# Kernel optimization log

Measured on AMD Instinct MI355X. Metric: run time of the kernel, lower is better.

## Reference

```python
import jax, jax.numpy as jnp
from jax import lax
import numpy as np

# ---- init hyperparameters (from init_kwargs) ----
STRIDE = 1
DP_CHANNELS = 1
ATOM_R = 8
ATOM_C = 8
NUMB_ATOM = 128
T_SC = 3
K = 256
BATCH = 32
IMG = 64


def setup_inputs() -> dict:
    key = jax.random.key(0)
    k1, k2 = jax.random.split(key)
    Y = jax.random.normal(k1, (BATCH, DP_CHANNELS, IMG, IMG), dtype=jnp.float32)
    # ConvTranspose2d weight layout: (numb_atom, dp_channels, atom_c, atom_r)
    W = jax.random.normal(k2, (NUMB_ATOM, DP_CHANNELS, ATOM_C, ATOM_R), dtype=jnp.float32)
    # normalise_weights(): each (i, j) filter divided by its L2 norm
    W = W / jnp.sqrt(jnp.sum(W ** 2, axis=(2, 3), keepdims=True))
    return {"Y": Y, "W_D": W}


def _conv_D(X, W):
    # PyTorch ConvTranspose2d (stride=1, no padding): full convolution with
    # spatially-flipped kernel; W is (in=numb_atom, out=dp_channels, kh, kw).
    kh, kw = W.shape[2], W.shape[3]
    return lax.conv_general_dilated(
        X, jnp.flip(W, (2, 3)), (1, 1),
        [(kh - 1, kh - 1), (kw - 1, kw - 1)],
        dimension_numbers=('NCHW', 'IOHW', 'NCHW'))


def _conv_Dt(R, Wt):
    # PyTorch Conv2d (VALID, stride=1): Wt is (out=numb_atom, in=dp, kh, kw)
    return lax.conv_general_dilated(
        R, Wt, (1, 1), 'VALID', dimension_numbers=('NCHW', 'OIHW', 'NCHW'))


def _hard_threshold_k(X, k):
    # keep the k largest-|.| entries per sample (over flattened C,H,W)
    B = X.shape[0]
    flat = X.reshape(B, -1)
    _, idx = lax.top_k(jnp.abs(flat), k)                      # [B, k]
    vals = jnp.take_along_axis(flat, idx, axis=1)             # [B, k]
    out = jnp.zeros_like(flat).at[jnp.arange(B)[:, None], idx].set(vals)
    return out.reshape(X.shape)


def _linesearch(Y, X, W, Wt, k):
    R = Y - _conv_D(X, W)
    g = _conv_Dt(R, Wt)
    l2_start = jnp.sum(R ** 2)

    def attempt(alpha):
        Xu = _hard_threshold_k(X + alpha * g, k)
        err = jnp.sum((Y - _conv_D(Xu, W)) ** 2)
        return Xu, err

    Xu0, err0 = attempt(jnp.float32(1.0))

    def cond(s):
        _, _, err, count = s
        return (err >= l2_start) & (count <= 15)

    def body(s):
        alpha, _, _, count = s
        alpha = alpha * jnp.float32(0.5)
        Xu, err = attempt(alpha)
        return (alpha, Xu, err, count + 1)

    alpha, Xu, err, _ = lax.while_loop(
        cond, body, (jnp.float32(1.0), Xu0, err0, jnp.int32(0)))
    return Xu, err, alpha


def reference(Y, W_D):
    # D_trans.weight = D.weight.permute(0,1,3,2) -> (numb_atom, dp, atom_r, atom_c)
    Wt = jnp.swapaxes(W_D, 2, 3)
    kh, kw = Wt.shape[2], Wt.shape[3]
    B, _, H, W_sp = Y.shape
    X = jnp.zeros((B, W_D.shape[0], H - kh + 1, W_sp - kw + 1), dtype=Y.dtype)
    for _ in range(T_SC):
        X, _, _ = _linesearch(Y, X, W_D, Wt, K)
    return X
```

## Files before the change

### kernel.cpp

```cpp
#include <hip/hip_runtime.h>
#include <stdint.h>

#define NB   32
#define NCH  128
#define IMG  64
#define IMG2 4096
#define OH   57
#define OHW  3249
#define CHW  415872
#define KTOP 256
#define NATT 17
#define NS   32
#define SCAP 512
#define NCAP 1536
#define NBUCK 8192
#define HSHIFT 18
#define TGT  512
#define RSTRIDE 72
#define NZB  257
#define BMW  12996

typedef unsigned long long ull;

__global__ void k_init(int* support_cnt) {
    if (threadIdx.x < NB) support_cnt[threadIdx.x] = 0;
}

__global__ __launch_bounds__(256) void k_resid(
    const float* __restrict__ Y, const float* __restrict__ W,
    const int* __restrict__ support_cnt, const uint32_t* __restrict__ support_idx,
    const float* __restrict__ support_val, float* __restrict__ Rg, double* __restrict__ l2part,
    uint32_t* __restrict__ hist, int* __restrict__ cand_cnt)
{
    int bx = blockIdx.x, tid = threadIdx.x;
    if (bx >= NB) {
        int zb = bx - NB;
        if (zb < 256) {
            ((uint4*)hist)[zb * 256 + tid] = make_uint4(0u, 0u, 0u, 0u);
        } else {
            ((uint4*)cand_cnt)[tid] = make_uint4(0u, 0u, 0u, 0u);
        }
        return;
    }
    int b = bx;
    __shared__ float Rs[IMG2];
    const float4* Y4 = (const float4*)(Y + b * IMG2);
    float4* R4 = (float4*)Rs;
    for (int i = tid; i < IMG2 / 4; i += 256) R4[i] = Y4[i];
    __syncthreads();
    int n = support_cnt[b];
    for (int task = tid; task < n * 64; task += 256) {
        int i = task >> 6, tap = task & 63, p = tap >> 3, q = tap & 7;
        uint32_t idx = support_idx[b * KTOP + i];
        float val = support_val[b * KTOP + i];
        int c = idx / OHW, rem = idx % OHW, s = rem / OH, t = rem % OH;
        float w = W[c * 64 + p * 8 + q];
        atomicAdd(&Rs[(s + p) * IMG + (t + q)], -val * w);
    }
    __syncthreads();
    double acc = 0.0;
    for (int i = tid; i < IMG2; i += 256) {
        float v = Rs[i];
        Rg[b * IMG2 + i] = v;
        acc += (double)v * (double)v;
    }
    __shared__ double red[256];
    red[tid] = acc; __syncthreads();
    for (int s2 = 128; s2 > 0; s2 >>= 1) { if (tid < s2) red[tid] += red[tid + s2]; __syncthreads(); }
    if (tid == 0) l2part[b] = red[0];
}

__global__ __launch_bounds__(256) void k_conv(
    const float* __restrict__ Rg, const float* __restrict__ W,
    float* __restrict__ g_out, uint32_t* __restrict__ hist)
{
    int b = blockIdx.x, cg0 = blockIdx.y, tid = threadIdx.x;
    __shared__ float Rs[71 * 72];
    __shared__ uint32_t hl[NBUCK];
    for (int i = tid; i < 71 * 72; i += 256) Rs[i] = 0.f;
    for (int i = tid; i < NBUCK; i += 256) hl[i] = 0u;
    __syncthreads();
    const float4* R4 = (const float4*)(Rg + b * IMG2);
    for (int i = tid; i < 1024; i += 256) {
        int row = i >> 4, col4 = (i & 15) * 4;
        *(float4*)&Rs[row * 72 + col4] = R4[i];
    }
    __syncthreads();
    int csub = tid >> 7;
    int tile = tid & 127;
    bool active = tile < 120;
    int tr = active ? tile / 15 : 0;
    int tc = active ? tile % 15 : 0;
    int s0 = tr * 8, t0 = tc * 4;

    for (int sub = 0; sub < 4; ++sub) {
        int c = cg0 * 8 + sub * 2 + csub;
        int c_s = __builtin_amdgcn_readfirstlane(c);
        const float* Wc = W + c_s * 64;

        float acc[8][4];
#pragma unroll
        for (int r = 0; r < 8; ++r)
#pragma unroll
            for (int cc = 0; cc < 4; ++cc) acc[r][cc] = 0.f;

#pragma unroll
        for (int rho = 0; rho < 15; ++rho) {
            float rb[12];
            const float* rp = &Rs[(s0 + rho) * 72 + t0];
            *(float4*)&rb[0] = *(const float4*)rp;
            *(float4*)&rb[4] = *(const float4*)(rp + 4);
            *(float4*)&rb[8] = *(const float4*)(rp + 8);
#pragma unroll
            for (int r = 0; r < 8; ++r) {
                const int p = rho - r;
                if (p >= 0 && p < 8) {
#pragma unroll
                    for (int q = 0; q < 8; ++q) {
                        float wv = Wc[q * 8 + p];
#pragma unroll
                        for (int cc = 0; cc < 4; ++cc)
                            acc[r][cc] = fmaf(rb[cc + q], wv, acc[r][cc]);
                    }
                }
            }
        }
        if (active) {
            float* go = g_out + (size_t)(b * NCH + c) * OHW;
#pragma unroll
            for (int r = 0; r < 8; ++r) {
                int s = s0 + r;
                if (s < OH) {
#pragma unroll
                    for (int cc = 0; cc < 4; ++cc) {
                        int t = t0 + cc;
                        if (t < OH) {
                            float v = acc[r][cc];
                            go[s * OH + t] = v;
                            uint32_t bits = __float_as_uint(v) & 0x7fffffffu;
                            atomicAdd(&hl[bits >> HSHIFT], 1u);
                        }
                    }
                }
            }
        }
    }
    __syncthreads();
    for (int i = tid; i < NBUCK; i += 256) {
        uint32_t v = hl[i];
        if (v) atomicAdd(&hist[b * NBUCK + i], v);
    }
}

__global__ __launch_bounds__(256) void k_thresh(const uint32_t* __restrict__ hist,
                                                uint32_t* __restrict__ thr) {
    int b = blockIdx.x, tid = threadIdx.x;
    uint32_t h[32];
    uint32_t s = 0;
    const uint32_t* hb = hist + b * NBUCK + tid * 32;
#pragma unroll
    for (int k = 0; k < 32; ++k) { h[k] = hb[k]; s += h[k]; }
    __shared__ uint32_t buf[2][256];
    int cur = 0;
    buf[0][tid] = s;
    __syncthreads();
    for (int d = 1; d < 256; d <<= 1) {
        uint32_t v = buf[cur][tid];
        if (tid + d < 256) v += buf[cur][tid + d];
        buf[cur ^ 1][tid] = v;
        cur ^= 1;
        __syncthreads();
    }
    uint32_t sufme = buf[cur][tid];
    uint32_t base  = (tid < 255) ? buf[cur][tid + 1] : 0u;
    if (tid == 0 && buf[cur][0] < TGT) thr[b] = 0u;
    if (base < TGT && sufme >= TGT) {
        uint32_t acc = base; int bk = 0;
#pragma unroll
        for (int k = 31; k >= 0; --k) {
            acc += h[k];
            if (acc >= TGT) { bk = tid * 32 + k; break; }
        }
        thr[b] = (uint32_t)bk << HSHIFT;
    }
}

__global__ __launch_bounds__(256) void k_collect(
    const float* __restrict__ g, const uint32_t* __restrict__ thr,
    int* __restrict__ cand_cnt, uint32_t* __restrict__ cand_idx, float* __restrict__ cand_g)
{
    int b = blockIdx.y;
    int i4 = blockIdx.x * 256 + threadIdx.x;
    if (i4 >= CHW / 4) return;
    int slice = blockIdx.x & (NS - 1);
    uint32_t tb = thr[b];
    float4 v4 = ((const float4*)(g + (size_t)b * CHW))[i4];
    float vv[4] = { v4.x, v4.y, v4.z, v4.w };
#pragma unroll
    for (int k = 0; k < 4; ++k) {
        uint32_t bits = __float_as_uint(vv[k]) & 0x7fffffffu;
        if (bits >= tb) {
            int pos = atomicAdd(&cand_cnt[b * NS + slice], 1);
            if (pos < SCAP) {
                cand_idx[(b * NS + slice) * SCAP + pos] = (uint32_t)(i4 * 4 + k);
                cand_g[(b * NS + slice) * SCAP + pos] = vv[k];
            }
        }
    }
}

__global__ __launch_bounds__(1024) void k_suppg(
    const float* __restrict__ g,
    const int* __restrict__ support_cnt, const uint32_t* __restrict__ support_idx,
    const int* __restrict__ cand_cnt, const uint32_t* __restrict__ cand_idx,
    const float* __restrict__ cand_g,
    uint32_t* __restrict__ ns_idx, float* __restrict__ ns_g, uint32_t* __restrict__ ns_pk,
    float* __restrict__ sup_g, uint32_t* __restrict__ sup_pk)
{
    int b = blockIdx.x, tid = threadIdx.x, lane = tid & 63;
    __shared__ uint32_t bm[BMW];
    __shared__ int cnts[NS];
    __shared__ ull ck[NCAP];
    __shared__ float cg_l[NCAP];
    __shared__ int nns_sh;
    int n = support_cnt[b];
    for (int i = tid; i < BMW / 4; i += 1024) ((uint4*)bm)[i] = make_uint4(0u, 0u, 0u, 0u);
    if (tid < NS) cnts[tid] = min(cand_cnt[b * NS + tid], SCAP);
    if (tid == 0) nns_sh = 0;
    __syncthreads();
    if (tid < KTOP) {
        if (tid < n) {
            uint32_t idx = support_idx[b * KTOP + tid];
            atomicOr(&bm[idx >> 5], 1u << (idx & 31));
            float gv = g[(size_t)b * CHW + idx];
            sup_g[b * KTOP + tid] = gv;
            int c = idx / OHW, r = idx % OHW, s = r / OH, t = r % OH;
            sup_pk[b * KTOP + tid] = (uint32_t)((c << 12) | (s << 6) | t);
        } else {
            sup_g[b * KTOP + tid] = 0.f;
            sup_pk[b * KTOP + tid] = 0u;
        }
    }
    __syncthreads();
    for (int t0 = tid; t0 < NS * SCAP; t0 += 1024) {
        int s = t0 >> 9, j = t0 & (SCAP - 1);
        bool keep = false; uint32_t idx = 0; float gv = 0.f;
        if (j < cnts[s]) {
            idx = cand_idx[(b * NS + s) * SCAP + j];
            gv = cand_g[(b * NS + s) * SCAP + j];
            keep = ((bm[idx >> 5] >> (idx & 31)) & 1u) == 0u;
        }
        ull mk = __ballot(keep);
        if (mk) {
            int basep = 0;
            if (lane == 0) basep = atomicAdd(&nns_sh, (int)__popcll(mk));
            basep = __shfl(basep, 0, 64);
            if (keep) {
                int p = basep + (int)__popcll(mk & ((1ull << lane) - 1ull));
                if (p < NCAP) {
                    ck[p] = ((ull)(__float_as_uint(gv) & 0x7fffffffu) << 32) | (ull)(uint32_t)(~idx);
                    cg_l[p] = gv;
                }
            }
        }
    }
    __syncthreads();
    int nns = min(nns_sh, NCAP);
    int nns8 = (nns + 7) & ~7;
    for (int i = nns + tid; i < nns8; i += 1024) ck[i] = 0ull;
    __syncthreads();
    ull myk[2]; int myr[2];
#pragma unroll
    for (int q = 0; q < 2; ++q) { int i = tid + 1024 * q; myk[q] = (i < nns) ? ck[i] : 0ull; myr[q] = 0; }
    for (int j = 0; j < nns8; j += 8) {
        ull t0 = ck[j], t1 = ck[j+1], t2 = ck[j+2], t3 = ck[j+3];
        ull t4 = ck[j+4], t5 = ck[j+5], t6 = ck[j+6], t7 = ck[j+7];
#pragma unroll
        for (int q = 0; q < 2; ++q) {
            myr[q] += ((t0 > myk[q]) ? 1 : 0) + ((t1 > myk[q]) ? 1 : 0)
                    + ((t2 > myk[q]) ? 1 : 0) + ((t3 > myk[q]) ? 1 : 0)
                    + ((t4 > myk[q]) ? 1 : 0) + ((t5 > myk[q]) ? 1 : 0)
                    + ((t6 > myk[q]) ? 1 : 0) + ((t7 > myk[q]) ? 1 : 0);
        }
    }
#pragma unroll
    for (int q = 0; q < 2; ++q) {
        int i = tid + 1024 * q;
        if (i < nns && myr[q] < KTOP) {
            uint32_t idx = ~(uint32_t)myk[q];
            int r = myr[q];
            ns_idx[b * KTOP + r] = idx;
            ns_g[b * KTOP + r] = cg_l[i];
            int c = idx / OHW, rr = idx % OHW, s = rr / OH, t = rr % OH;
            ns_pk[b * KTOP + r] = (uint32_t)((c << 12) | (s << 6) | t);
        }
    }
}

__global__ __launch_bounds__(512) void k_att2(
    const float* __restrict__ Y, const float* __restrict__ W,
    const int* __restrict__ support_cnt, const uint32_t* __restrict__ support_idx,
    const float* __restrict__ support_val,
    const float* __restrict__ sup_g, const uint32_t* __restrict__ sup_pk,
    const uint32_t* __restrict__ ns_idx, const float* __restrict__ ns_g,
    const uint32_t* __restrict__ ns_pk,
    uint32_t* __restrict__ sel_idx, float* __restrict__ sel_val, double* __restrict__ err)
{
    int a = blockIdx.x, b = blockIdx.y, tid = threadIdx.x;
    int lane = tid & 63, wid = tid >> 6;
    float alpha = ldexpf(1.f, -a);
    int n = support_cnt[b];

    __shared__ float recon[64 * RSTRIDE];
    __shared__ ull kA[KTOP];
    __shared__ ull kB[KTOP];
    __shared__ float s_v[KTOP];
    __shared__ uint32_t s_pk2[KTOP];
    __shared__ double redd[8];

    uint32_t myi = 0, mypk = 0;
    float myv = 0.f;
    ull myk = 0;
    if (tid < KTOP) {
        myi = ns_idx[b * KTOP + tid];
        myv = alpha * ns_g[b * KTOP + tid];
        mypk = ns_pk[b * KTOP + tid];
        myk = ((ull)(__float_as_uint(myv) & 0x7fffffffu) << 32) | (ull)(uint32_t)(~myi);
        kA[tid] = myk;
    } else {
        int t2 = tid - KTOP;
        if (t2 < n) {
            myi = support_idx[b * KTOP + t2];
            myv = fmaf(alpha, sup_g[b * KTOP + t2], support_val[b * KTOP + t2]);
            mypk = sup_pk[b * KTOP + t2];
        } else {
            myi = (uint32_t)(CHW + t2);
            myv = 0.f; mypk = 0u;
        }
        myk = ((ull)(__float_as_uint(myv) & 0x7fffffffu) << 32) | (ull)(uint32_t)(~myi);
        kB[t2] = myk;
    }
    for (int i = tid; i < 64 * RSTRIDE; i += 512) recon[i] = 0.f;
    __syncthreads();

    int cb = 0;
    for (int j = 0; j < KTOP; j += 8) {
        ull t0 = kB[j], t1 = kB[j+1], t2 = kB[j+2], t3 = kB[j+3];
        ull t4 = kB[j+4], t5 = kB[j+5], t6 = kB[j+6], t7 = kB[j+7];
        cb += ((t0 > myk) ? 1 : 0) + ((t1 > myk) ? 1 : 0)
            + ((t2 > myk) ? 1 : 0) + ((t3 > myk) ? 1 : 0)
            + ((t4 > myk) ? 1 : 0) + ((t5 > myk) ? 1 : 0)
            + ((t6 > myk) ? 1 : 0) + ((t7 > myk) ? 1 : 0);
    }
    int rank;
    if (tid < KTOP) {
        rank = tid + cb;
    } else {
        int lo = 0, hi = KTOP;
        while (lo < hi) { int mid = (lo + hi) >> 1; if (kA[mid] > myk) lo = mid + 1; else hi = mid; }
        rank = lo + cb;
    }
    size_t o = ((size_t)a * NB + b) * KTOP;
    if (rank < KTOP) {
        s_v[rank] = myv; s_pk2[rank] = mypk;
        sel_idx[o + rank] = myi; sel_val[o + rank] = myv;
    }
    __syncthreads();

#pragma unroll 4
    for (int task = tid; task < KTOP * 64; task += 512) {
        int i = task >> 6, tap = task & 63, p = tap >> 3, q = tap & 7;
        uint32_t pk = s_pk2[i];
        float val = s_v[i];
        int c = pk >> 12, s = (pk >> 6) & 63, t = pk & 63;
        atomicAdd(&recon[(s + p) * RSTRIDE + (t + q)], val * W[c * 64 + tap]);
    }
    __syncthreads();

    const float4* Y4 = (const float4*)(Y + b * IMG2);
    double accd = 0.0;
#pragma unroll
    for (int q2 = 0; q2 < 2; ++q2) {
        int idx = tid * 2 + q2;
        float4 y4 = Y4[idx];
        int row = idx >> 4, col = (idx & 15) * 4;
        const float* rr = &recon[row * RSTRIDE + col];
        float d0 = y4.x - rr[0]; accd += (double)d0 * (double)d0;
        float d1 = y4.y - rr[1]; accd += (double)d1 * (double)d1;
        float d2 = y4.z - rr[2]; accd += (double)d2 * (double)d2;
        float d3 = y4.w - rr[3]; accd += (double)d3 * (double)d3;
    }
    for (int d = 32; d > 0; d >>= 1) accd += __shfl_xor(accd, d, 64);
    if (lane == 0) redd[wid] = accd;
    __syncthreads();
    if (tid == 0) {
        double e = 0.0;
#pragma unroll
        for (int w2 = 0; w2 < 8; ++w2) e += redd[w2];
        err[a * NB + b] = e;
    }
}

__global__ __launch_bounds__(256) void k_update(
    const double* __restrict__ l2part, const double* __restrict__ err,
    const uint32_t* __restrict__ sel_idx, const float* __restrict__ sel_val,
    int* __restrict__ support_cnt, uint32_t* __restrict__ support_idx, float* __restrict__ support_val)
{
    int b = blockIdx.x, tid = threadIdx.x;
    __shared__ double esum[NATT + 1];
    __shared__ int sel_sh;
    if (tid < NATT) {
        double e = 0.0;
        for (int b2 = 0; b2 < NB; ++b2) e += err[tid * NB + b2];
        esum[tid] = e;
    } else if (tid == NATT) {
        double l2 = 0.0;
        for (int b2 = 0; b2 < NB; ++b2) l2 += l2part[b2];
        esum[NATT] = l2;
    }
    __syncthreads();
    if (tid == 0) {
        double l2 = esum[NATT];
        int sel = NATT - 1;
        for (int a2 = 0; a2 < NATT; ++a2) if (esum[a2] < l2) { sel = a2; break; }
        sel_sh = sel;
    }
    __syncthreads();
    int a = sel_sh;
    __shared__ uint32_t ki[KTOP];
    __shared__ float kv[KTOP];
    ki[tid] = sel_idx[((size_t)a * NB + b) * KTOP + tid];
    kv[tid] = sel_val[((size_t)a * NB + b) * KTOP + tid];
    __syncthreads();
    uint32_t me = ki[tid];
    int rank = 0;
    for (int j = 0; j < KTOP; j += 8) {
        uint32_t a0 = ki[j], a1 = ki[j+1], a2 = ki[j+2], a3 = ki[j+3];
        uint32_t a4 = ki[j+4], a5 = ki[j+5], a6 = ki[j+6], a7 = ki[j+7];
        rank += ((a0 < me) ? 1 : 0) + ((a1 < me) ? 1 : 0) + ((a2 < me) ? 1 : 0) + ((a3 < me) ? 1 : 0)
              + ((a4 < me) ? 1 : 0) + ((a5 < me) ? 1 : 0) + ((a6 < me) ? 1 : 0) + ((a7 < me) ? 1 : 0);
    }
    support_idx[b * KTOP + rank] = me;
    support_val[b * KTOP + rank] = kv[tid];
    if (tid == 0) support_cnt[b] = KTOP;
}

__global__ void k_outzero(float4* __restrict__ out) {
    int i = blockIdx.x * 256 + threadIdx.x;
    if (i < (NB * CHW) / 4) out[i] = make_float4(0.f, 0.f, 0.f, 0.f);
}

__global__ void k_scatter(const uint32_t* __restrict__ support_idx, const float* __restrict__ support_val,
                          float* __restrict__ out) {
    int b = blockIdx.x, tid = threadIdx.x;
    if (tid < KTOP) out[(size_t)b * CHW + support_idx[b * KTOP + tid]] = support_val[b * KTOP + tid];
}

static size_t align256(size_t x) { return (x + 255) & ~(size_t)255; }

extern "C" void kernel_launch(void* const* d_in, const int* in_sizes, int n_in,
                              void* d_out, int out_size, void* d_ws, size_t ws_size,
                              hipStream_t stream)
{
    const float* Y = (const float*)d_in[0];
    const float* W = (const float*)d_in[1];
    float* out = (float*)d_out;

    char* p = (char*)d_ws;
    size_t off = 0;
    auto carve = [&](size_t bytes) { void* r = p + off; off = align256(off + bytes); return r; };
    float*    Rg          = (float*)   carve(NB * IMG2 * sizeof(float));
    uint32_t* hist        = (uint32_t*)carve((size_t)NB * NBUCK * sizeof(uint32_t));
    uint32_t* thr         = (uint32_t*)carve(NB * sizeof(uint32_t));
    int*      cand_cnt    = (int*)     carve(NB * NS * sizeof(int));
    double*   l2part      = (double*)  carve(NB * sizeof(double));
    double*   err         = (double*)  carve(NATT * NB * sizeof(double));
    int*      support_cnt = (int*)     carve(NB * sizeof(int));
    uint32_t* support_idx = (uint32_t*)carve(NB * KTOP * sizeof(uint32_t));
    float*    support_val = (float*)   carve(NB * KTOP * sizeof(float));
    uint32_t* sel_idx     = (uint32_t*)carve((size_t)NATT * NB * KTOP * sizeof(uint32_t));
    float*    sel_val     = (float*)   carve((size_t)NATT * NB * KTOP * sizeof(float));
    uint32_t* cand_idx    = (uint32_t*)carve((size_t)NB * NS * SCAP * sizeof(uint32_t));
    float*    cand_g      = (float*)   carve((size_t)NB * NS * SCAP * sizeof(float));
    uint32_t* ns_idx      = (uint32_t*)carve(NB * KTOP * sizeof(uint32_t));
    float*    ns_gbuf     = (float*)   carve(NB * KTOP * sizeof(float));
    uint32_t* ns_pk       = (uint32_t*)carve(NB * KTOP * sizeof(uint32_t));
    float*    sup_gbuf    = (float*)   carve(NB * KTOP * sizeof(float));
    uint32_t* sup_pk      = (uint32_t*)carve(NB * KTOP * sizeof(uint32_t));
    (void)ws_size; (void)in_sizes; (void)n_in; (void)out_size;

    k_init<<<1, 64, 0, stream>>>(support_cnt);
    for (int t = 0; t < 3; ++t) {
        k_resid<<<NB + NZB, 256, 0, stream>>>(Y, W, support_cnt, support_idx, support_val,
                                              Rg, l2part, hist, cand_cnt);
        k_conv<<<dim3(NB, 16), 256, 0, stream>>>(Rg, W, out, hist);
        k_thresh<<<NB, 256, 0, stream>>>(hist, thr);
        k_collect<<<dim3((CHW / 4 + 255) / 256, NB), 256, 0, stream>>>(out, thr, cand_cnt, cand_idx, cand_g);
        k_suppg<<<NB, 1024, 0, stream>>>(out, support_cnt, support_idx,
                                         cand_cnt, cand_idx, cand_g,
                                         ns_idx, ns_gbuf, ns_pk, sup_gbuf, sup_pk);
        k_att2<<<dim3(NATT, NB), 512, 0, stream>>>(Y, W, support_cnt, support_idx, support_val,
                                                   sup_gbuf, sup_pk, ns_idx, ns_gbuf, ns_pk,
                                                   sel_idx, sel_val, err);
        k_update<<<NB, 256, 0, stream>>>(l2part, err, sel_idx, sel_val,
                                         support_cnt, support_idx, support_val);
    }
    k_outzero<<<((NB * CHW) / 4 + 255) / 256, 256, 0, stream>>>((float4*)out);
    k_scatter<<<NB, 256, 0, stream>>>(support_idx, support_val, out);
}
```

Measured before the change: 663.3 us.

## Pack support and candidate arrays into wide structs and reshape attempt kernel

Merges the separate index, value and packed-coordinate arrays into 64-bit and uint4 records so each element is read with one wide load. The attempt kernel also changes: the rank count uses wavefront shuffles instead of LDS reads, Y is prefetched before the scatter phase, and the reconstruction scatter is restructured so each wave handles one support element with 64 taps and software-prefetches the weights. The sel_idx/sel_val writes move to after the reduction. Wide packing adds some padding bytes, and the shuffle loop may cost more instructions than the LDS broadcast reads.

```diff
diff --git a/kernel.cpp b/kernel.cpp
--- a/kernel.cpp
+++ b/kernel.cpp
@@ -28,8 +28,8 @@
 
 __global__ __launch_bounds__(256) void k_resid(
     const float* __restrict__ Y, const float* __restrict__ W,
-    const int* __restrict__ support_cnt, const uint32_t* __restrict__ support_idx,
-    const float* __restrict__ support_val, float* __restrict__ Rg, double* __restrict__ l2part,
+    const int* __restrict__ support_cnt, const ull* __restrict__ sup_iv,
+    float* __restrict__ Rg, double* __restrict__ l2part,
     uint32_t* __restrict__ hist, int* __restrict__ cand_cnt)
 {
     int bx = blockIdx.x, tid = threadIdx.x;
@@ -51,8 +51,9 @@
     int n = support_cnt[b];
     for (int task = tid; task < n * 64; task += 256) {
         int i = task >> 6, tap = task & 63, p = tap >> 3, q = tap & 7;
-        uint32_t idx = support_idx[b * KTOP + i];
-        float val = support_val[b * KTOP + i];
+        ull iv = sup_iv[b * KTOP + i];
+        uint32_t idx = (uint32_t)iv;
+        float val = __uint_as_float((uint32_t)(iv >> 32));
         int c = idx / OHW, rem = idx % OHW, s = rem / OH, t = rem % OH;
         float w = W[c * 64 + p * 8 + q];
         atomicAdd(&Rs[(s + p) * IMG + (t + q)], -val * w);
@@ -211,11 +212,10 @@
 
 __global__ __launch_bounds__(1024) void k_suppg(
     const float* __restrict__ g,
-    const int* __restrict__ support_cnt, const uint32_t* __restrict__ support_idx,
+    const int* __restrict__ support_cnt, const ull* __restrict__ sup_iv,
     const int* __restrict__ cand_cnt, const uint32_t* __restrict__ cand_idx,
     const float* __restrict__ cand_g,
-    uint32_t* __restrict__ ns_idx, float* __restrict__ ns_g, uint32_t* __restrict__ ns_pk,
-    float* __restrict__ sup_g, uint32_t* __restrict__ sup_pk)
+    uint4* __restrict__ ns_pack, ull* __restrict__ sup_gp)
 {
     int b = blockIdx.x, tid = threadIdx.x, lane = tid & 63;
     __shared__ uint32_t bm[BMW];
@@ -230,15 +230,14 @@
     __syncthreads();
     if (tid < KTOP) {
         if (tid < n) {
-            uint32_t idx = support_idx[b * KTOP + tid];
+            uint32_t idx = (uint32_t)sup_iv[b * KTOP + tid];
             atomicOr(&bm[idx >> 5], 1u << (idx & 31));
             float gv = g[(size_t)b * CHW + idx];
-            sup_g[b * KTOP + tid] = gv;
             int c = idx / OHW, r = idx % OHW, s = r / OH, t = r % OH;
-            sup_pk[b * KTOP + tid] = (uint32_t)((c << 12) | (s << 6) | t);
+            uint32_t pk = (uint32_t)((c << 12) | (s << 6) | t);
+            sup_gp[b * KTOP + tid] = ((ull)__float_as_uint(gv) << 32) | (ull)pk;
         } else {
-            sup_g[b * KTOP + tid] = 0.f;
-            sup_pk[b * KTOP + tid] = 0u;
+            sup_gp[b * KTOP + tid] = 0ull;
         }
     }
     __syncthreads();
@@ -289,21 +288,17 @@
         if (i < nns && myr[q] < KTOP) {
             uint32_t idx = ~(uint32_t)myk[q];
             int r = myr[q];
-            ns_idx[b * KTOP + r] = idx;
-            ns_g[b * KTOP + r] = cg_l[i];
             int c = idx / OHW, rr = idx % OHW, s = rr / OH, t = rr % OH;
-            ns_pk[b * KTOP + r] = (uint32_t)((c << 12) | (s << 6) | t);
+            uint32_t pk = (uint32_t)((c << 12) | (s << 6) | t);
+            ns_pack[b * KTOP + r] = make_uint4(idx, __float_as_uint(cg_l[i]), pk, 0u);
         }
     }
 }
 
 __global__ __launch_bounds__(512) void k_att2(
     const float* __restrict__ Y, const float* __restrict__ W,
-    const int* __restrict__ support_cnt, const uint32_t* __restrict__ support_idx,
-    const float* __restrict__ support_val,
-    const float* __restrict__ sup_g, const uint32_t* __restrict__ sup_pk,
-    const uint32_t* __restrict__ ns_idx, const float* __restrict__ ns_g,
-    const uint32_t* __restrict__ ns_pk,
+    const int* __restrict__ support_cnt, const ull* __restrict__ sup_iv,
+    const ull* __restrict__ sup_gp, const uint4* __restrict__ ns_pack,
     uint32_t* __restrict__ sel_idx, float* __restrict__ sel_val, double* __restrict__ err)
 {
     int a = blockIdx.x, b = blockIdx.y, tid = threadIdx.x;
@@ -314,25 +309,29 @@
     __shared__ float recon[64 * RSTRIDE];
     __shared__ ull kA[KTOP];
     __shared__ ull kB[KTOP];
-    __shared__ float s_v[KTOP];
-    __shared__ uint32_t s_pk2[KTOP];
+    __shared__ ull s_pv[KTOP];
+    __shared__ uint32_t s_idx[KTOP];
     __shared__ double redd[8];
 
     uint32_t myi = 0, mypk = 0;
     float myv = 0.f;
     ull myk = 0;
     if (tid < KTOP) {
-        myi = ns_idx[b * KTOP + tid];
-        myv = alpha * ns_g[b * KTOP + tid];
-        mypk = ns_pk[b * KTOP + tid];
+        uint4 np = ns_pack[b * KTOP + tid];
+        myi = np.x;
+        myv = alpha * __uint_as_float(np.y);
+        mypk = np.z;
         myk = ((ull)(__float_as_uint(myv) & 0x7fffffffu) << 32) | (ull)(uint32_t)(~myi);
         kA[tid] = myk;
     } else {
         int t2 = tid - KTOP;
+        ull gp = sup_gp[b * KTOP + t2];
+        ull iv = sup_iv[b * KTOP + t2];
         if (t2 < n) {
-            myi = support_idx[b * KTOP + t2];
-            myv = fmaf(alpha, sup_g[b * KTOP + t2], support_val[b * KTOP + t2]);
-            mypk = sup_pk[b * KTOP + t2];
+            myi = (uint32_t)iv;
+            myv = fmaf(alpha, __uint_as_float((uint32_t)(gp >> 32)),
+                       __uint_as_float((uint32_t)(iv >> 32)));
+            mypk = (uint32_t)gp;
         } else {
             myi = (uint32_t)(CHW + t2);
             myv = 0.f; mypk = 0u;
@@ -340,17 +339,21 @@
         myk = ((ull)(__float_as_uint(myv) & 0x7fffffffu) << 32) | (ull)(uint32_t)(~myi);
         kB[t2] = myk;
     }
+
+    const float4* Y4 = (const float4*)(Y + b * IMG2);
+    float4 y0 = Y4[tid * 2], y1 = Y4[tid * 2 + 1];
+
     for (int i = tid; i < 64 * RSTRIDE; i += 512) recon[i] = 0.f;
     __syncthreads();
 
+    ull kb0 = kB[lane], kb1 = kB[64 + lane], kb2 = kB[128 + lane], kb3 = kB[192 + lane];
     int cb = 0;
-    for (int j = 0; j < KTOP; j += 8) {
-        ull t0 = kB[j], t1 = kB[j+1], t2 = kB[j+2], t3 = kB[j+3];
-        ull t4 = kB[j+4], t5 = kB[j+5], t6 = kB[j+6], t7 = kB[j+7];
-        cb += ((t0 > myk) ? 1 : 0) + ((t1 > myk) ? 1 : 0)
-            + ((t2 > myk) ? 1 : 0) + ((t3 > myk) ? 1 : 0)
-            + ((t4 > myk) ? 1 : 0) + ((t5 > myk) ? 1 : 0)
-            + ((t6 > myk) ? 1 : 0) + ((t7 > myk) ? 1 : 0);
+#pragma unroll
+    for (int l = 0; l < 64; ++l) {
+        ull o0 = __shfl(kb0, l, 64); cb += (o0 > myk) ? 1 : 0;
+        ull o1 = __shfl(kb1, l, 64); cb += (o1 > myk) ? 1 : 0;
+        ull o2 = __shfl(kb2, l, 64); cb += (o2 > myk) ? 1 : 0;
+        ull o3 = __shfl(kb3, l, 64); cb += (o3 > myk) ? 1 : 0;
     }
     int rank;
     if (tid < KTOP) {
@@ -360,35 +363,55 @@
         while (lo < hi) { int mid = (lo + hi) >> 1; if (kA[mid] > myk) lo = mid + 1; else hi = mid; }
         rank = lo + cb;
     }
-    size_t o = ((size_t)a * NB + b) * KTOP;
     if (rank < KTOP) {
-        s_v[rank] = myv; s_pk2[rank] = mypk;
-        sel_idx[o + rank] = myi; sel_val[o + rank] = myv;
-    }
-    __syncthreads();
-
-#pragma unroll 4
-    for (int task = tid; task < KTOP * 64; task += 512) {
-        int i = task >> 6, tap = task & 63, p = tap >> 3, q = tap & 7;
-        uint32_t pk = s_pk2[i];
-        float val = s_v[i];
-        int c = pk >> 12, s = (pk >> 6) & 63, t = pk & 63;
-        atomicAdd(&recon[(s + p) * RSTRIDE + (t + q)], val * W[c * 64 + tap]);
-    }
-    __syncthreads();
-
-    const float4* Y4 = (const float4*)(Y + b * IMG2);
+        s_pv[rank] = ((ull)__float_as_uint(myv) << 32) | (ull)mypk;
+        s_idx[rank] = myi;
+    }
+    __syncthreads();
+
+    {
+        int p = lane >> 3, q = lane & 7;
+        ull pv[4]; float wv[4];
+#pragma unroll
+        for (int j = 0; j < 4; ++j) pv[j] = s_pv[wid + 8 * j];
+#pragma unroll
+        for (int j = 0; j < 4; ++j) wv[j] = W[(((uint32_t)pv[j]) >> 12) * 64 + lane];
+#pragma unroll
+        for (int k4 = 0; k4 < 32; k4 += 4) {
+            ull npv[4] = {0, 0, 0, 0}; float nwv[4] = {0.f, 0.f, 0.f, 0.f};
+            if (k4 + 4 < 32) {
+#pragma unroll
+                for (int j = 0; j < 4; ++j) npv[j] = s_pv[wid + 8 * (k4 + 4 + j)];
+#pragma unroll
+                for (int j = 0; j < 4; ++j) nwv[j] = W[(((uint32_t)npv[j]) >> 12) * 64 + lane];
+            }
+#pragma unroll
+            for (int j = 0; j < 4; ++j) {
+                uint32_t pk = (uint32_t)pv[j];
+                float val = __uint_as_float((uint32_t)(pv[j] >> 32));
+                int s = (pk >> 6) & 63, t = pk & 63;
+                atomicAdd(&recon[(s + p) * RSTRIDE + (t + q)], val * wv[j]);
+            }
+#pragma unroll
+            for (int j = 0; j < 4; ++j) { pv[j] = npv[j]; wv[j] = nwv[j]; }
+        }
+    }
+    __syncthreads();
+
     double accd = 0.0;
-#pragma unroll
-    for (int q2 = 0; q2 < 2; ++q2) {
-        int idx = tid * 2 + q2;
-        float4 y4 = Y4[idx];
-        int row = idx >> 4, col = (idx & 15) * 4;
-        const float* rr = &recon[row * RSTRIDE + col];
-        float d0 = y4.x - rr[0]; accd += (double)d0 * (double)d0;
-        float d1 = y4.y - rr[1]; accd += (double)d1 * (double)d1;
-        float d2 = y4.z - rr[2]; accd += (double)d2 * (double)d2;
-        float d3 = y4.w - rr[3]; accd += (double)d3 * (double)d3;
+    {
+        int idx0 = tid * 2;
+        const float* rr = &recon[(idx0 >> 4) * RSTRIDE + (idx0 & 15) * 4];
+        float d0 = y0.x - rr[0]; accd += (double)d0 * (double)d0;
+        float d1 = y0.y - rr[1]; accd += (double)d1 * (double)d1;
+        float d2 = y0.z - rr[2]; accd += (double)d2 * (double)d2;
+        float d3 = y0.w - rr[3]; accd += (double)d3 * (double)d3;
+        int idx1 = tid * 2 + 1;
+        rr = &recon[(idx1 >> 4) * RSTRIDE + (idx1 & 15) * 4];
+        float e0 = y1.x - rr[0]; accd += (double)e0 * (double)e0;
+        float e1 = y1.y - rr[1]; accd += (double)e1 * (double)e1;
+        float e2 = y1.z - rr[2]; accd += (double)e2 * (double)e2;
+        float e3 = y1.w - rr[3]; accd += (double)e3 * (double)e3;
     }
     for (int d = 32; d > 0; d >>= 1) accd += __shfl_xor(accd, d, 64);
     if (lane == 0) redd[wid] = accd;
@@ -398,13 +421,20 @@
 #pragma unroll
         for (int w2 = 0; w2 < 8; ++w2) e += redd[w2];
         err[a * NB + b] = e;
+    }
+
+    if (tid < KTOP) {
+        size_t o = ((size_t)a * NB + b) * KTOP;
+        ull pvt = s_pv[tid];
+        sel_idx[o + tid] = s_idx[tid];
+        sel_val[o + tid] = __uint_as_float((uint32_t)(pvt >> 32));
     }
 }
 
 __global__ __launch_bounds__(256) void k_update(
     const double* __restrict__ l2part, const double* __restrict__ err,
     const uint32_t* __restrict__ sel_idx, const float* __restrict__ sel_val,
-    int* __restrict__ support_cnt, uint32_t* __restrict__ support_idx, float* __restrict__ support_val)
+    int* __restrict__ support_cnt, ull* __restrict__ sup_iv)
 {
     int b = blockIdx.x, tid = threadIdx.x;
     __shared__ double esum[NATT + 1];
@@ -440,8 +470,7 @@
         rank += ((a0 < me) ? 1 : 0) + ((a1 < me) ? 1 : 0) + ((a2 < me) ? 1 : 0) + ((a3 < me) ? 1 : 0)
               + ((a4 < me) ? 1 : 0) + ((a5 < me) ? 1 : 0) + ((a6 < me) ? 1 : 0) + ((a7 < me) ? 1 : 0);
     }
-    support_idx[b * KTOP + rank] = me;
-    support_val[b * KTOP + rank] = kv[tid];
+    sup_iv[b * KTOP + rank] = (ull)me | ((ull)__float_as_uint(kv[tid]) << 32);
     if (tid == 0) support_cnt[b] = KTOP;
 }
 
@@ -450,10 +479,12 @@
     if (i < (NB * CHW) / 4) out[i] = make_float4(0.f, 0.f, 0.f, 0.f);
 }
 
-__global__ void k_scatter(const uint32_t* __restrict__ support_idx, const float* __restrict__ support_val,
-                          float* __restrict__ out) {
+__global__ void k_scatter(const ull* __restrict__ sup_iv, float* __restrict__ out) {
     int b = blockIdx.x, tid = threadIdx.x;
-    if (tid < KTOP) out[(size_t)b * CHW + support_idx[b * KTOP + tid]] = support_val[b * KTOP + tid];
+    if (tid < KTOP) {
+        ull iv = sup_iv[b * KTOP + tid];
+        out[(size_t)b * CHW + (uint32_t)iv] = __uint_as_float((uint32_t)(iv >> 32));
+    }
 }
 
 static size_t align256(size_t x) { return (x + 255) & ~(size_t)255; }
@@ -476,35 +507,31 @@
     double*   l2part      = (double*)  carve(NB * sizeof(double));
     double*   err         = (double*)  carve(NATT * NB * sizeof(double));
     int*      support_cnt = (int*)     carve(NB * sizeof(int));
-    uint32_t* support_idx = (uint32_t*)carve(NB * KTOP * sizeof(uint32_t));
-    float*    support_val = (float*)   carve(NB * KTOP * sizeof(float));
+    ull*      sup_iv      = (ull*)     carve((size_t)NB * KTOP * sizeof(ull));
     uint32_t* sel_idx     = (uint32_t*)carve((size_t)NATT * NB * KTOP * sizeof(uint32_t));
     float*    sel_val     = (float*)   carve((size_t)NATT * NB * KTOP * sizeof(float));
     uint32_t* cand_idx    = (uint32_t*)carve((size_t)NB * NS * SCAP * sizeof(uint32_t));
     float*    cand_g      = (float*)   carve((size_t)NB * NS * SCAP * sizeof(float));
-    uint32_t* ns_idx      = (uint32_t*)carve(NB * KTOP * sizeof(uint32_t));
-    float*    ns_gbuf     = (float*)   carve(NB * KTOP * sizeof(float));
-    uint32_t* ns_pk       = (uint32_t*)carve(NB * KTOP * sizeof(uint32_t));
-    float*    sup_gbuf    = (float*)   carve(NB * KTOP * sizeof(float));
-    uint32_t* sup_pk      = (uint32_t*)carve(NB * KTOP * sizeof(uint32_t));
+    uint4*    ns_pack     = (uint4*)   carve((size_t)NB * KTOP * sizeof(uint4));
+    ull*      sup_gp      = (ull*)     carve((size_t)NB * KTOP * sizeof(ull));
     (void)ws_size; (void)in_sizes; (void)n_in; (void)out_size;
 
     k_init<<<1, 64, 0, stream>>>(support_cnt);
     for (int t = 0; t < 3; ++t) {
-        k_resid<<<NB + NZB, 256, 0, stream>>>(Y, W, support_cnt, support_idx, support_val,
+        k_resid<<<NB + NZB, 256, 0, stream>>>(Y, W, support_cnt, sup_iv,
                                               Rg, l2part, hist, cand_cnt);
         k_conv<<<dim3(NB, 16), 256, 0, stream>>>(Rg, W, out, hist);
         k_thresh<<<NB, 256, 0, stream>>>(hist, thr);
         k_collect<<<dim3((CHW / 4 + 255) / 256, NB), 256, 0, stream>>>(out, thr, cand_cnt, cand_idx, cand_g);
-        k_suppg<<<NB, 1024, 0, stream>>>(out, support_cnt, support_idx,
+        k_suppg<<<NB, 1024, 0, stream>>>(out, support_cnt, sup_iv,
                                          cand_cnt, cand_idx, cand_g,
-                                         ns_idx, ns_gbuf, ns_pk, sup_gbuf, sup_pk);
-        k_att2<<<dim3(NATT, NB), 512, 0, stream>>>(Y, W, support_cnt, support_idx, support_val,
-                                                   sup_gbuf, sup_pk, ns_idx, ns_gbuf, ns_pk,
+                                         ns_pack, sup_gp);
+        k_att2<<<dim3(NATT, NB), 512, 0, stream>>>(Y, W, support_cnt, sup_iv,
+                                                   sup_gp, ns_pack,
                                                    sel_idx, sel_val, err);
         k_update<<<NB, 256, 0, stream>>>(l2part, err, sel_idx, sel_val,
-                                         support_cnt, support_idx, support_val);
+                                         support_cnt, sup_iv);
     }
     k_outzero<<<((NB * CHW) / 4 + 255) / 256, 256, 0, stream>>>((float4*)out);
-    k_scatter<<<NB, 256, 0, stream>>>(support_idx, support_val, out);
-}
+    k_scatter<<<NB, 256, 0, stream>>>(sup_iv, out);
+}
```

Measured after the change: 1.189 ms. +79.2%, slower.
